# Kernel tuning notes

Hardware: AMD Instinct MI355X
Metric: run time of the kernel (lower is better)

Reference implementation:

```python
import math
import jax, jax.numpy as jnp
import numpy as np

HEADS = 8


def setup_inputs() -> dict:
    key = jax.random.key(0)
    k1, k2 = jax.random.split(key)
    b, heads, c, t, s_enc = 4, HEADS, 64, 1024, 1024
    x = jax.random.normal(k1, (b, 3 * heads * c, t), dtype=jnp.float32)
    encoder_kv = jax.random.normal(k2, (b, 2 * heads * c, s_enc), dtype=jnp.float32)
    return {"x": x, "encoder_kv": encoder_kv}


def reference(x, encoder_kv):
    heads = HEADS
    b, ch3, t = x.shape
    c = ch3 // (3 * heads)
    s_enc = encoder_kv.shape[-1]
    # 'b (qkv heads c) h -> qkv (b heads) c h'
    qkv = x.reshape(b, 3, heads, c, t).transpose(1, 0, 2, 3, 4).reshape(3, b * heads, c, t)
    q, k, v = qkv[0], qkv[1], qkv[2]
    ekv = encoder_kv.reshape(b, 2, heads, c, s_enc).transpose(1, 0, 2, 3, 4).reshape(2, b * heads, c, s_enc)
    ek, ev = ekv[0], ekv[1]
    k = jnp.concatenate([ek, k], axis=-1)  # (bh, c, s_enc + t)
    v = jnp.concatenate([ev, v], axis=-1)
    scale = 1.0 / math.sqrt(math.sqrt(c))
    weight = jnp.einsum('bct,bcs->bts', q * scale, k * scale)  # (bh, t, s)
    weight = jax.nn.softmax(weight.astype(jnp.float32), axis=-1).astype(weight.dtype)
    out = jnp.einsum('bts,bcs->bct', weight, v)  # (bh, c, t)
    # '(b heads) c h -> b (heads c) h'
    out = out.reshape(b, heads, c, t).reshape(b, heads * c, t)
    return out
```

## Files before the change

### kernel.cpp

```cpp
#include <hip/hip_runtime.h>

typedef __attribute__((ext_vector_type(8))) short bf16x8;
typedef __attribute__((ext_vector_type(16))) float f32x16;
typedef __attribute__((ext_vector_type(4))) float f32x4;
typedef __attribute__((ext_vector_type(4))) unsigned int u32x4;

#define NH 8
#define CD 64
#define TLEN 1024
#define SENC 1024
#define STOT 2048
#define NGRP 4
#define KRANGE (STOT / NGRP)
#define SKG 32
#define NITG (KRANGE / SKG)
#define BQ 64
#define QSCALE 0.18033688f

__device__ __forceinline__ ushort f2bf(float f) {
  uint x = __builtin_bit_cast(uint, f);
  uint r = (x + 0x7fffu + ((x >> 16) & 1u)) >> 16;
  return (ushort)r;
}
__device__ __forceinline__ uint4 pack8(const ushort* p) {
  uint4 u;
  u.x = (uint)p[0] | ((uint)p[1] << 16);
  u.y = (uint)p[2] | ((uint)p[3] << 16);
  u.z = (uint)p[4] | ((uint)p[5] << 16);
  u.w = (uint)p[6] | ((uint)p[7] << 16);
  return u;
}
__device__ __forceinline__ uint cvtpk(float lo, float hi) {
  uint r;
  asm("v_cvt_pk_bf16_f32 %0, %1, %2" : "=v"(r) : "v"(lo), "v"(hi));
  return r;
}
__device__ __forceinline__ void plswap(uint& a, uint& b) {
  asm("v_permlane32_swap_b32 %0, %1" : "+v"(a), "+v"(b));
}
__device__ __forceinline__ bf16x8 mk8(uint a, uint b, uint c, uint d) {
  u32x4 t = {a, b, c, d};
  return __builtin_bit_cast(bf16x8, t);
}

__global__ __launch_bounds__(256)
void repack_kernel(const float* __restrict__ x, const float* __restrict__ ekv,
                   ushort* __restrict__ ktw, ushort* __restrict__ vnw) {
  const int kx = blockIdx.x;
  const int bh = blockIdx.y;
  const int b = bh >> 3, h = bh & 7;
  const int t = threadIdx.x;
  const float* ks;
  const float* vs;
  if (kx < 16) {
    ks = ekv + (size_t)(b * 2 * NH * CD + h * CD) * SENC + kx * 64;
    vs = ekv + (size_t)(b * 2 * NH * CD + NH * CD + h * CD) * SENC + kx * 64;
  } else {
    ks = x + (size_t)(b * 3 * NH * CD + NH * CD + h * CD) * TLEN + (kx - 16) * 64;
    vs = x + (size_t)(b * 3 * NH * CD + 2 * NH * CD + h * CD) * TLEN + (kx - 16) * 64;
  }
  if (blockIdx.z == 0) {
    __shared__ float Lt[64 * 65];
    const int ci = t >> 2, seg = t & 3;
#pragma unroll
    for (int j = 0; j < 4; ++j) {
      float4 d = *(const float4*)&ks[ci * 1024 + seg * 16 + 4 * j];
      Lt[ci * 65 + seg * 16 + 4 * j + 0] = d.x;
      Lt[ci * 65 + seg * 16 + 4 * j + 1] = d.y;
      Lt[ci * 65 + seg * 16 + 4 * j + 2] = d.z;
      Lt[ci * 65 + seg * 16 + 4 * j + 3] = d.w;
    }
    __syncthreads();
    const int key = t >> 2;
    ushort tmp[16];
#pragma unroll
    for (int u = 0; u < 16; ++u)
      tmp[u] = f2bf(Lt[(seg * 16 + u) * 65 + key]);
    ushort* dst = ktw + ((size_t)bh * STOT + kx * 64 + key) * CD + seg * 16;
    *(uint4*)dst = pack8(tmp);
    *(uint4*)(dst + 8) = pack8(tmp + 8);
  } else {
    const int ci = t >> 2, seg = t & 3;
    ushort tmp[16];
#pragma unroll
    for (int j = 0; j < 4; ++j) {
      float4 d = *(const float4*)&vs[ci * 1024 + seg * 16 + 4 * j];
      tmp[4 * j + 0] = f2bf(d.x);
      tmp[4 * j + 1] = f2bf(d.y);
      tmp[4 * j + 2] = f2bf(d.z);
      tmp[4 * j + 3] = f2bf(d.w);
    }
    ushort* dst = vnw + (size_t)bh * CD * STOT + (size_t)ci * STOT + kx * 64 + seg * 16;
    *(uint4*)dst = pack8(tmp);
    *(uint4*)(dst + 8) = pack8(tmp + 8);
  }
}

__global__ __launch_bounds__(512, 4)
void qkv_attn_ws(const float* __restrict__ x, const ushort* __restrict__ ktw,
                 const ushort* __restrict__ vnw, float* __restrict__ out) {
  __shared__ __align__(16) ushort arena[NGRP * 2 * 2 * SKG * CD];

  const int tid  = threadIdx.x;
  const int w    = tid >> 6;
  const int qcol = w & 1;
  const int grp  = w >> 1;
  const int lane = tid & 63;
  const int al   = lane & 31;
  const int h    = lane >> 5;
  const int tg   = tid & 127;

  const int f  = blockIdx.x;
  const int bh = (f & 7) | (((f >> 7) & 3) << 3);
  const int qt = (f >> 3) & 15;
  const int b  = bh >> 3;
  const int hh = bh & 7;
  const int t0 = qt * BQ;
  const int kbase = grp * KRANGE;

  const float* qg = x + (size_t)(b * 3 * NH * CD + hh * CD) * TLEN;
  float* og = out + (size_t)(b * NH * CD + hh * CD) * TLEN;
  const ushort* ktb = ktw + (size_t)bh * STOT * CD;
  const ushort* vnb = vnw + (size_t)bh * CD * STOT;

  ushort* Kg[2]; ushort* Vg[2];
#pragma unroll
  for (int buf = 0; buf < 2; ++buf) {
    Kg[buf] = arena + (size_t)((grp * 2 + buf) * 2 + 0) * (SKG * CD);
    Vg[buf] = arena + (size_t)((grp * 2 + buf) * 2 + 1) * (SKG * CD);
  }

  const int krow = tg >> 2;
  const int kcb  = (tg & 3) * 2;
  const int kswz0 = ((kcb + 0) ^ (krow & 7)) * 8;
  const int kswz1 = ((kcb + 1) ^ (krow & 7)) * 8;
  const int vrow = tg >> 1;
  const int vcb  = (tg & 1) * 2;
  const int vswz0 = ((vcb + 0) ^ ((vrow >> 1) & 3)) * 8;
  const int vswz1 = ((vcb + 1) ^ ((vrow >> 1) & 3)) * 8;

  uint4 kp0 = *(const uint4*)(ktb + (size_t)(kbase + krow) * CD + (kcb + 0) * 8);
  uint4 kp1 = *(const uint4*)(ktb + (size_t)(kbase + krow) * CD + (kcb + 1) * 8);
  uint4 vp0 = *(const uint4*)(vnb + (size_t)vrow * STOT + kbase + (vcb + 0) * 8);
  uint4 vp1 = *(const uint4*)(vnb + (size_t)vrow * STOT + kbase + (vcb + 1) * 8);
  *(uint4*)&Kg[0][krow * CD + kswz0] = kp0;
  *(uint4*)&Kg[0][krow * CD + kswz1] = kp1;
  *(uint4*)&Vg[0][vrow * SKG + vswz0] = vp0;
  *(uint4*)&Vg[0][vrow * SKG + vswz1] = vp1;

  const int q_l = qcol * 32 + al;
  const float* qp = qg + t0 + q_l;
  float qv[4][8];
#pragma unroll
  for (int kst = 0; kst < 4; ++kst)
#pragma unroll
    for (int j = 0; j < 8; ++j)
      qv[kst][j] = qp[(size_t)(kst * 16 + h * 8 + j) * TLEN] * QSCALE;
  bf16x8 qfrag[4];
#pragma unroll
  for (int kst = 0; kst < 4; ++kst)
    qfrag[kst] = mk8(cvtpk(qv[kst][0], qv[kst][1]), cvtpk(qv[kst][2], qv[kst][3]),
                     cvtpk(qv[kst][4], qv[kst][5]), cvtpk(qv[kst][6], qv[kst][7]));

  __syncthreads();

  int koff[4];
#pragma unroll
  for (int kst = 0; kst < 4; ++kst) koff[kst] = ((2 * kst + h) ^ (al & 7)) * 8;
  const int vx = (al >> 1) & 3;
  int voff[2];
#pragma unroll
  for (int kst = 0; kst < 2; ++kst) voff[kst] = ((2 * kst + h) ^ vx) * 8;

  f32x16 of0, of1;
#pragma unroll
  for (int i = 0; i < 16; ++i) { of0[i] = 0.f; of1[i] = 0.f; }
  float l_acc = 0.f;

  for (int it = 0; it < NITG; ++it) {
    const int cur = it & 1;

    if (it + 1 < NITG) {
      const int s1 = kbase + (it + 1) * SKG;
      kp0 = *(const uint4*)(ktb + (size_t)(s1 + krow) * CD + (kcb + 0) * 8);
      kp1 = *(const uint4*)(ktb + (size_t)(s1 + krow) * CD + (kcb + 1) * 8);
      vp0 = *(const uint4*)(vnb + (size_t)vrow * STOT + s1 + (vcb + 0) * 8);
      vp1 = *(const uint4*)(vnb + (size_t)vrow * STOT + s1 + (vcb + 1) * 8);
    }

    const ushort* kt = Kg[cur];
    const ushort* vt = Vg[cur];

    f32x16 acc;
#pragma unroll
    for (int i = 0; i < 16; ++i) acc[i] = 0.f;
#pragma unroll
    for (int kst = 0; kst < 4; ++kst) {
      bf16x8 afr = *(const bf16x8*)&kt[al * CD + koff[kst]];
      acc = __builtin_amdgcn_mfma_f32_32x32x16_bf16(afr, qfrag[kst], acc, 0, 0, 0);
    }
    uint ulo[4], uhi[4];
#pragma unroll
    for (int rq = 0; rq < 4; ++rq) {
      float p0 = exp2f(acc[4 * rq + 0]);
      float p1 = exp2f(acc[4 * rq + 1]);
      float p2 = exp2f(acc[4 * rq + 2]);
      float p3 = exp2f(acc[4 * rq + 3]);
      l_acc += (p0 + p1) + (p2 + p3);
      ulo[rq] = cvtpk(p0, p1);
      uhi[rq] = cvtpk(p2, p3);
    }

    bf16x8 pfr[2];
#pragma unroll
    for (int kst = 0; kst < 2; ++kst) {
      uint xlo = ulo[2 * kst], ylo = ulo[2 * kst + 1];
      uint xhi = uhi[2 * kst], yhi = uhi[2 * kst + 1];
      plswap(xlo, ylo);
      plswap(xhi, yhi);
      pfr[kst] = mk8(xlo, xhi, ylo, yhi);
    }

#pragma unroll
    for (int kst = 0; kst < 2; ++kst) {
      bf16x8 v0 = *(const bf16x8*)&vt[(0 * 32 + al) * SKG + voff[kst]];
      bf16x8 v1 = *(const bf16x8*)&vt[(1 * 32 + al) * SKG + voff[kst]];
      of0 = __builtin_amdgcn_mfma_f32_32x32x16_bf16(v0, pfr[kst], of0, 0, 0, 0);
      of1 = __builtin_amdgcn_mfma_f32_32x32x16_bf16(v1, pfr[kst], of1, 0, 0, 0);
    }

    if (it + 1 < NITG) {
      const int nb = cur ^ 1;
      *(uint4*)&Kg[nb][krow * CD + kswz0] = kp0;
      *(uint4*)&Kg[nb][krow * CD + kswz1] = kp1;
      *(uint4*)&Vg[nb][vrow * SKG + vswz0] = vp0;
      *(uint4*)&Vg[nb][vrow * SKG + vswz1] = vp1;
      __syncthreads();
    }
  }

  __syncthreads();
  float* fa = (float*)arena;
  float* tA = fa;
  float* tB = fa + 64 * 68;
  float* lf = fa + 2 * 64 * 68;
  float lv = l_acc + __shfl_xor(l_acc, 32);
  if (h == 0) lf[grp * 64 + q_l] = lv;

  if (grp >= 2) {
    float* T = (grp == 2) ? tA : tB;
#pragma unroll
    for (int rq = 0; rq < 4; ++rq) {
      *(f32x4*)&T[q_l * 68 + 8 * rq + 4 * h] =
          f32x4{of0[4 * rq + 0], of0[4 * rq + 1], of0[4 * rq + 2], of0[4 * rq + 3]};
      *(f32x4*)&T[q_l * 68 + 32 + 8 * rq + 4 * h] =
          f32x4{of1[4 * rq + 0], of1[4 * rq + 1], of1[4 * rq + 2], of1[4 * rq + 3]};
    }
  }
  __syncthreads();
  if (grp < 2) {
    const float* T = (grp == 0) ? tA : tB;
#pragma unroll
    for (int rq = 0; rq < 4; ++rq) {
      f32x4 a = *(const f32x4*)&T[q_l * 68 + 8 * rq + 4 * h];
      f32x4 c = *(const f32x4*)&T[q_l * 68 + 32 + 8 * rq + 4 * h];
#pragma unroll
      for (int j = 0; j < 4; ++j) { of0[4 * rq + j] += a[j]; of1[4 * rq + j] += c[j]; }
    }
  }
  __syncthreads();
  if (grp == 1) {
#pragma unroll
    for (int rq = 0; rq < 4; ++rq) {
      *(f32x4*)&tA[q_l * 68 + 8 * rq + 4 * h] =
          f32x4{of0[4 * rq + 0], of0[4 * rq + 1], of0[4 * rq + 2], of0[4 * rq + 3]};
      *(f32x4*)&tA[q_l * 68 + 32 + 8 * rq + 4 * h] =
          f32x4{of1[4 * rq + 0], of1[4 * rq + 1], of1[4 * rq + 2], of1[4 * rq + 3]};
    }
  }
  __syncthreads();
  if (grp == 0) {
#pragma unroll
    for (int rq = 0; rq < 4; ++rq) {
      f32x4 a = *(const f32x4*)&tA[q_l * 68 + 8 * rq + 4 * h];
      f32x4 c = *(const f32x4*)&tA[q_l * 68 + 32 + 8 * rq + 4 * h];
#pragma unroll
      for (int j = 0; j < 4; ++j) { of0[4 * rq + j] += a[j]; of1[4 * rq + j] += c[j]; }
    }
    float lsum = lf[q_l] + lf[64 + q_l] + lf[128 + q_l] + lf[192 + q_l];
    float inv = 1.0f / lsum;
    float* ob = og + t0 + q_l;
#pragma unroll
    for (int r = 0; r < 16; ++r) {
      int ci = (r & 3) + 8 * (r >> 2) + 4 * h;
      ob[(size_t)ci * TLEN] = of0[r] * inv;
      ob[(size_t)(32 + ci) * TLEN] = of1[r] * inv;
    }
  }
}

extern "C" void kernel_launch(void* const* d_in, const int* in_sizes, int n_in,
                              void* d_out, int out_size, void* d_ws, size_t ws_size,
                              hipStream_t stream) {
  const float* x   = (const float*)d_in[0];
  const float* ekv = (const float*)d_in[1];
  float* out = (float*)d_out;
  ushort* ktw = (ushort*)d_ws;
  ushort* vnw = ktw + (size_t)32 * STOT * CD;
  repack_kernel<<<dim3(32, 32, 2), 256, 0, stream>>>(x, ekv, ktw, vnw);
  qkv_attn_ws<<<32 * 16, 512, 0, stream>>>(x, ktw, vnw, out);
}
```

Baseline: 123.3 us.

## Load K/V MFMA fragments directly from global memory, drop LDS staging

New measurement: 142.1 us. 1.15x slower.

```diff
diff --git a/kernel.cpp b/kernel.cpp
--- a/kernel.cpp
+++ b/kernel.cpp
@@ -99,7 +99,7 @@
 __global__ __launch_bounds__(512, 4)
 void qkv_attn_ws(const float* __restrict__ x, const ushort* __restrict__ ktw,
                  const ushort* __restrict__ vnw, float* __restrict__ out) {
-  __shared__ __align__(16) ushort arena[NGRP * 2 * 2 * SKG * CD];
+  __shared__ float fa[8960];
 
   const int tid  = threadIdx.x;
   const int w    = tid >> 6;
@@ -108,7 +108,6 @@
   const int lane = tid & 63;
   const int al   = lane & 31;
   const int h    = lane >> 5;
-  const int tg   = tid & 127;
 
   const int f  = blockIdx.x;
   const int bh = (f & 7) | (((f >> 7) & 3) << 3);
@@ -123,30 +122,9 @@
   const ushort* ktb = ktw + (size_t)bh * STOT * CD;
   const ushort* vnb = vnw + (size_t)bh * CD * STOT;
 
-  ushort* Kg[2]; ushort* Vg[2];
-#pragma unroll
-  for (int buf = 0; buf < 2; ++buf) {
-    Kg[buf] = arena + (size_t)((grp * 2 + buf) * 2 + 0) * (SKG * CD);
-    Vg[buf] = arena + (size_t)((grp * 2 + buf) * 2 + 1) * (SKG * CD);
-  }
-
-  const int krow = tg >> 2;
-  const int kcb  = (tg & 3) * 2;
-  const int kswz0 = ((kcb + 0) ^ (krow & 7)) * 8;
-  const int kswz1 = ((kcb + 1) ^ (krow & 7)) * 8;
-  const int vrow = tg >> 1;
-  const int vcb  = (tg & 1) * 2;
-  const int vswz0 = ((vcb + 0) ^ ((vrow >> 1) & 3)) * 8;
-  const int vswz1 = ((vcb + 1) ^ ((vrow >> 1) & 3)) * 8;
-
-  uint4 kp0 = *(const uint4*)(ktb + (size_t)(kbase + krow) * CD + (kcb + 0) * 8);
-  uint4 kp1 = *(const uint4*)(ktb + (size_t)(kbase + krow) * CD + (kcb + 1) * 8);
-  uint4 vp0 = *(const uint4*)(vnb + (size_t)vrow * STOT + kbase + (vcb + 0) * 8);
-  uint4 vp1 = *(const uint4*)(vnb + (size_t)vrow * STOT + kbase + (vcb + 1) * 8);
-  *(uint4*)&Kg[0][krow * CD + kswz0] = kp0;
-  *(uint4*)&Kg[0][krow * CD + kswz1] = kp1;
-  *(uint4*)&Vg[0][vrow * SKG + vswz0] = vp0;
-  *(uint4*)&Vg[0][vrow * SKG + vswz1] = vp1;
+  const ushort* kfp = ktb + (size_t)(kbase + al) * CD + h * 8;
+  const ushort* vq0 = vnb + (size_t)(0 * 32 + al) * STOT + kbase + h * 8;
+  const ushort* vq1 = vnb + (size_t)(1 * 32 + al) * STOT + kbase + h * 8;
 
   const int q_l = qcol * 32 + al;
   const float* qp = qg + t0 + q_l;
@@ -162,43 +140,33 @@
     qfrag[kst] = mk8(cvtpk(qv[kst][0], qv[kst][1]), cvtpk(qv[kst][2], qv[kst][3]),
                      cvtpk(qv[kst][4], qv[kst][5]), cvtpk(qv[kst][6], qv[kst][7]));
 
-  __syncthreads();
-
-  int koff[4];
-#pragma unroll
-  for (int kst = 0; kst < 4; ++kst) koff[kst] = ((2 * kst + h) ^ (al & 7)) * 8;
-  const int vx = (al >> 1) & 3;
-  int voff[2];
-#pragma unroll
-  for (int kst = 0; kst < 2; ++kst) voff[kst] = ((2 * kst + h) ^ vx) * 8;
-
   f32x16 of0, of1;
 #pragma unroll
   for (int i = 0; i < 16; ++i) { of0[i] = 0.f; of1[i] = 0.f; }
   float l_acc = 0.f;
 
+#pragma unroll 2
   for (int it = 0; it < NITG; ++it) {
-    const int cur = it & 1;
-
-    if (it + 1 < NITG) {
-      const int s1 = kbase + (it + 1) * SKG;
-      kp0 = *(const uint4*)(ktb + (size_t)(s1 + krow) * CD + (kcb + 0) * 8);
-      kp1 = *(const uint4*)(ktb + (size_t)(s1 + krow) * CD + (kcb + 1) * 8);
-      vp0 = *(const uint4*)(vnb + (size_t)vrow * STOT + s1 + (vcb + 0) * 8);
-      vp1 = *(const uint4*)(vnb + (size_t)vrow * STOT + s1 + (vcb + 1) * 8);
-    }
-
-    const ushort* kt = Kg[cur];
-    const ushort* vt = Vg[cur];
+    const ushort* kp = kfp + (size_t)it * SKG * CD;
+    const ushort* va = vq0 + it * SKG;
+    const ushort* vb = vq1 + it * SKG;
+    bf16x8 kf0 = *(const bf16x8*)(kp + 0);
+    bf16x8 kf1 = *(const bf16x8*)(kp + 16);
+    bf16x8 kf2 = *(const bf16x8*)(kp + 32);
+    bf16x8 kf3 = *(const bf16x8*)(kp + 48);
+    bf16x8 va0 = *(const bf16x8*)(va + 0);
+    bf16x8 va1 = *(const bf16x8*)(va + 16);
+    bf16x8 vb0 = *(const bf16x8*)(vb + 0);
+    bf16x8 vb1 = *(const bf16x8*)(vb + 16);
 
     f32x16 acc;
 #pragma unroll
     for (int i = 0; i < 16; ++i) acc[i] = 0.f;
-#pragma unroll
-    for (int kst = 0; kst < 4; ++kst) {
-      bf16x8 afr = *(const bf16x8*)&kt[al * CD + koff[kst]];
-      acc = __builtin_amdgcn_mfma_f32_32x32x16_bf16(afr, qfrag[kst], acc, 0, 0, 0);
-    }
+    acc = __builtin_amdgcn_mfma_f32_32x32x16_bf16(kf0, qfrag[0], acc, 0, 0, 0);
+    acc = __builtin_amdgcn_mfma_f32_32x32x16_bf16(kf1, qfrag[1], acc, 0, 0, 0);
+    acc = __builtin_amdgcn_mfma_f32_32x32x16_bf16(kf2, qfrag[2], acc, 0, 0, 0);
+    acc = __builtin_amdgcn_mfma_f32_32x32x16_bf16(kf3, qfrag[3], acc, 0, 0, 0);
+
     uint ulo[4], uhi[4];
 #pragma unroll
     for (int rq = 0; rq < 4; ++rq) {
@@ -221,26 +189,13 @@
       pfr[kst] = mk8(xlo, xhi, ylo, yhi);
     }
 
-#pragma unroll
-    for (int kst = 0; kst < 2; ++kst) {
-      bf16x8 v0 = *(const bf16x8*)&vt[(0 * 32 + al) * SKG + voff[kst]];
-      bf16x8 v1 = *(const bf16x8*)&vt[(1 * 32 + al) * SKG + voff[kst]];
-      of0 = __builtin_amdgcn_mfma_f32_32x32x16_bf16(v0, pfr[kst], of0, 0, 0, 0);
-      of1 = __builtin_amdgcn_mfma_f32_32x32x16_bf16(v1, pfr[kst], of1, 0, 0, 0);
-    }
-
-    if (it + 1 < NITG) {
-      const int nb = cur ^ 1;
-      *(uint4*)&Kg[nb][krow * CD + kswz0] = kp0;
-      *(uint4*)&Kg[nb][krow * CD + kswz1] = kp1;
-      *(uint4*)&Vg[nb][vrow * SKG + vswz0] = vp0;
-      *(uint4*)&Vg[nb][vrow * SKG + vswz1] = vp1;
-      __syncthreads();
-    }
-  }
-
-  __syncthreads();
-  float* fa = (float*)arena;
+    of0 = __builtin_amdgcn_mfma_f32_32x32x16_bf16(va0, pfr[0], of0, 0, 0, 0);
+    of0 = __builtin_amdgcn_mfma_f32_32x32x16_bf16(va1, pfr[1], of0, 0, 0, 0);
+    of1 = __builtin_amdgcn_mfma_f32_32x32x16_bf16(vb0, pfr[0], of1, 0, 0, 0);
+    of1 = __builtin_amdgcn_mfma_f32_32x32x16_bf16(vb1, pfr[1], of1, 0, 0, 0);
+  }
+
+  __syncthreads();
   float* tA = fa;
   float* tB = fa + 64 * 68;
   float* lf = fa + 2 * 64 * 68;
```
